# Optimization experiments

Measured on AMD Instinct MI355X. Metric: run time of the kernel, lower is better.

The kernel has to match this reference:

```python
import jax, jax.numpy as jnp
import numpy as np


def setup_inputs() -> dict:
    key = jax.random.key(0)
    k0, k1, k2, k3 = jax.random.split(key, 4)
    T, H, I, E, K = 2048, 2048, 1408, 8, 2  # tokens, hidden, intermediate, experts, top-k
    hidden_states = jax.random.normal(k0, (T, H), dtype=jnp.float32)
    router_weight = jax.random.normal(k1, (H, E), dtype=jnp.float32) * 0.02
    gate_up_weight = jax.random.normal(k2, (E, H, 2 * I), dtype=jnp.float32) * 0.02
    down_weight = jax.random.normal(k3, (E, I, H), dtype=jnp.float32) * 0.02
    return {
        "hidden_states": hidden_states,
        "router_weight": router_weight,
        "gate_up_weight": gate_up_weight,
        "down_weight": down_weight,
        "top_k": K,
    }


def reference(hidden_states, router_weight, gate_up_weight, down_weight, top_k):
    # Router: logits -> softmax -> top-k -> renormalize ('normalization' path)
    router_logits = hidden_states @ router_weight                  # [T, E]
    router_weights = jax.nn.softmax(router_logits, axis=-1)       # [T, E]
    topk_w, topk_idx = jax.lax.top_k(router_weights, top_k)       # [T, K]
    topk_w = topk_w / jnp.sum(topk_w, axis=-1, keepdims=True)     # router_weights_topk_reduced

    T, H = hidden_states.shape
    I = down_weight.shape[1]

    # Grouped gate_up GEMM (dense-per-expert reference for the grouped GMM)
    gate_up = jnp.einsum('th,ehf->etf', hidden_states, gate_up_weight)  # [E, T, 2I]
    gate, up = gate_up[..., :I], gate_up[..., I:]
    swish_out = jax.nn.silu(gate) * up                              # SWIGLU  [E, T, I]
    mlp_out = jnp.einsum('eti,eih->eth', swish_out, down_weight)    # [E, T, H]

    # Scatter-combine: gather each token's top-k expert outputs, weighted sum
    sel = mlp_out[topk_idx, jnp.arange(T)[:, None]]                 # [T, K, H]
    out = jnp.sum(sel * topk_w[..., None], axis=1)                  # [T, H]
    return out
```

## Files before the change

kernel.cpp:

```cpp
#include <hip/hip_runtime.h>
#include <hip/hip_bf16.h>
#include <math.h>

#define T_TOK 2048
#define HDIM  2048
#define IDIM  1408
#define NG    2816
#define NEXP  8
#define NPAIR (T_TOK*2)
#define RPAD  6144

typedef __attribute__((ext_vector_type(4))) float  f32x4;
typedef __attribute__((ext_vector_type(4))) short  s16x4;
typedef __attribute__((ext_vector_type(8))) short  s16x8;
typedef __attribute__((ext_vector_type(8))) __bf16 bf16x8;

__device__ __forceinline__ short f2bf(float f) {
  union { float f; unsigned u; } v; v.f = f;
  unsigned r = v.u + 0x7FFFu + ((v.u >> 16) & 1u);
  return (short)(r >> 16);
}

__device__ __forceinline__ float bf2f(short s) {
  union { unsigned u; float f; } v; v.u = ((unsigned)(unsigned short)s) << 16;
  return v.f;
}

__device__ __forceinline__ void gload_lds16(const void* g, void* l) {
  __builtin_amdgcn_global_load_lds((const __attribute__((address_space(1))) unsigned int*)g,
                                   (__attribute__((address_space(3))) unsigned int*)l,
                                   16, 0, 0);
}

__global__ void router_kernel(const float* __restrict__ hs, const float* __restrict__ rw,
                              int* __restrict__ pair_e, float* __restrict__ pair_w,
                              int* __restrict__ pair_pos, int* __restrict__ counts) {
  int wid = threadIdx.x >> 6, lane = threadIdx.x & 63;
  int t = blockIdx.x * 4 + wid;
  float acc[NEXP];
#pragma unroll
  for (int e = 0; e < NEXP; e++) acc[e] = 0.f;
  const float* h = hs + (size_t)t * HDIM;
  for (int k = lane; k < HDIM; k += 64) {
    float x = h[k];
    f32x4 w0 = *(const f32x4*)(rw + (size_t)k * NEXP);
    f32x4 w1 = *(const f32x4*)(rw + (size_t)k * NEXP + 4);
#pragma unroll
    for (int e = 0; e < 4; e++) { acc[e] += x * w0[e]; acc[e + 4] += x * w1[e]; }
  }
#pragma unroll
  for (int e = 0; e < NEXP; e++)
#pragma unroll
    for (int off = 32; off > 0; off >>= 1)
      acc[e] += __shfl_xor(acc[e], off, 64);
  if (lane == 0) {
    int i1 = 0; float v1 = acc[0];
#pragma unroll
    for (int e = 1; e < NEXP; e++) if (acc[e] > v1) { v1 = acc[e]; i1 = e; }
    int i2 = -1; float v2 = -3.4e38f;
#pragma unroll
    for (int e = 0; e < NEXP; e++) if (e != i1 && acc[e] > v2) { v2 = acc[e]; i2 = e; }
    float w2 = 1.f / (1.f + expf(v1 - v2));
    float w1 = 1.f - w2;
    int p1 = atomicAdd(&counts[i1], 1);
    int p2 = atomicAdd(&counts[i2], 1);
    pair_e[2*t]   = i1; pair_w[2*t]   = w1; pair_pos[2*t]   = p1;
    pair_e[2*t+1] = i2; pair_w[2*t+1] = w2; pair_pos[2*t+1] = p2;
  }
}

__global__ void prefix_kernel(const int* __restrict__ counts, int* __restrict__ offs) {
  if (threadIdx.x == 0) {
    int s = 0;
    for (int e = 0; e < NEXP; e++) { offs[e] = s; s += (counts[e] + 255) & ~255; }
    offs[NEXP] = s;
  }
}

__global__ void rowmap_kernel(const int* __restrict__ pair_e, const float* __restrict__ pair_w,
                              const int* __restrict__ pair_pos, const int* __restrict__ offs,
                              int* __restrict__ row_token, float* __restrict__ row_weight,
                              int* __restrict__ tok2row) {
  int p = blockIdx.x * 256 + threadIdx.x;
  if (p >= NPAIR) return;
  int e = pair_e[p];
  int row = offs[e] + pair_pos[p];
  row_token[row] = p >> 1;
  row_weight[row] = pair_w[p];
  tok2row[p] = row;
}

__global__ __launch_bounds__(256) void gather_kernel(const float* __restrict__ hs,
                                                     const int* __restrict__ row_token,
                                                     short* __restrict__ A_c) {
  int r = blockIdx.x;
  int tok = row_token[r];
  int t = threadIdx.x;
  if (tok < 0) {
    *(s16x8*)&A_c[(size_t)r * HDIM + t * 8] = (s16x8)0;
    return;
  }
  const float* src = hs + (size_t)tok * HDIM + t * 8;
  f32x4 v0 = *(const f32x4*)src;
  f32x4 v1 = *(const f32x4*)(src + 4);
  s16x8 o;
#pragma unroll
  for (int j = 0; j < 4; j++) { o[j] = f2bf(v0[j]); o[4 + j] = f2bf(v1[j]); }
  int dstg = (t & ~7) | ((t & 7) ^ (r & 7));
  *(s16x8*)&A_c[(size_t)r * HDIM + dstg * 8] = o;
}

__global__ __launch_bounds__(512, 2) void gateup_kernel(
    const short* __restrict__ A_c, const float* __restrict__ guw,
    const int* __restrict__ offs, short* __restrict__ S) {
  int nb = blockIdx.x;
  int rb = blockIdx.y * 256;
  if (rb >= offs[NEXP]) return;
  int e = 0;
#pragma unroll
  for (int i = 1; i < NEXP; i++) e += (rb >= offs[i]);
  const float* Wsrc = guw + (size_t)e * HDIM * NG;
  const short* Ar = A_c + (size_t)rb * HDIM;

  __shared__ short bufA[2][256 * 64];
  __shared__ short bufB[256 * 64];
  int tid = threadIdx.x, lane = tid & 63, wid = tid >> 6;
  int wm = wid >> 2, wn = wid & 3;
  int lm = lane & 15, lg = lane >> 4;

  int oct = tid >> 4, kq = tid & 15;
  int n0 = oct * 8;
  int col = (n0 < 128) ? (nb * 128 + n0) : (IDIM + nb * 128 + (n0 - 128));
  const float* Bp = Wsrc + col;

  f32x4 acc[8][4];
#pragma unroll
  for (int a = 0; a < 8; a++)
#pragma unroll
    for (int b = 0; b < 4; b++) acc[a][b] = (f32x4)0.f;

  f32x4 va[4], vb[4];

  auto STAGE_A = [&](int buf, int kt) {
    int k0 = kt * 64;
#pragma unroll
    for (int it = 0; it < 4; it++) {
      int idx = tid + it * 512;
      gload_lds16(Ar + (size_t)(idx >> 3) * HDIM + k0 + (idx & 7) * 8, &bufA[buf][idx * 8]);
    }
  };
  auto LOAD_B = [&](int kt) {
    const float* p = Bp + (size_t)(kt * 64 + kq * 4) * NG;
#pragma unroll
    for (int j = 0; j < 4; j++) {
      va[j] = *(const f32x4*)(p + (size_t)j * NG);
      vb[j] = *(const f32x4*)(p + (size_t)j * NG + 4);
    }
  };
  auto WRITE_B = [&]() {
    int gc = kq >> 1, half = kq & 1;
#pragma unroll
    for (int i = 0; i < 8; i++) {
      int n = n0 + i;
      s16x4 w;
#pragma unroll
      for (int j = 0; j < 4; j++) w[j] = f2bf(i < 4 ? va[j][i] : vb[j][i - 4]);
      *(s16x4*)&bufB[n * 64 + ((gc ^ (n & 7)) * 8) + half * 4] = w;
    }
  };

  STAGE_A(0, 0);
  LOAD_B(0);
  const int NT = HDIM / 64;
#pragma unroll 1
  for (int kt = 0; kt < NT; kt++) {
    int cur = kt & 1;
    if (kt + 1 < NT) {
      STAGE_A(cur ^ 1, kt + 1);
      asm volatile("s_waitcnt vmcnt(4)" ::: "memory");
    } else {
      asm volatile("s_waitcnt vmcnt(0)" ::: "memory");
    }
    WRITE_B();
    if (kt + 1 < NT) LOAD_B(kt + 1);
    asm volatile("s_waitcnt lgkmcnt(0)" ::: "memory");
    __builtin_amdgcn_s_barrier();
#pragma unroll
    for (int ks = 0; ks < 2; ks++) {
      bf16x8 a[8], b[4];
#pragma unroll
      for (int mi = 0; mi < 8; mi++) {
        int m = wm * 128 + mi * 16 + lm;
        a[mi] = *(const bf16x8*)&bufA[cur][m * 64 + (((ks * 4 + lg) ^ (m & 7)) * 8)];
      }
#pragma unroll
      for (int nf = 0; nf < 4; nf++) {
        int n = (nf >> 1) * 128 + wn * 32 + (nf & 1) * 16 + lm;
        b[nf] = *(const bf16x8*)&bufB[n * 64 + (((ks * 4 + lg) ^ (n & 7)) * 8)];
      }
      __builtin_amdgcn_s_setprio(1);
#pragma unroll
      for (int mi = 0; mi < 8; mi++)
#pragma unroll
        for (int nf = 0; nf < 4; nf++)
          acc[mi][nf] = __builtin_amdgcn_mfma_f32_16x16x32_bf16(a[mi], b[nf], acc[mi][nf], 0, 0, 0);
      __builtin_amdgcn_s_setprio(0);
    }
    asm volatile("s_waitcnt lgkmcnt(0)" ::: "memory");
    __builtin_amdgcn_s_barrier();
  }
#pragma unroll
  for (int mi = 0; mi < 8; mi++)
#pragma unroll
    for (int nfg = 0; nfg < 2; nfg++)
#pragma unroll
      for (int j = 0; j < 4; j++) {
        int row = wm * 128 + mi * 16 + lg * 4 + j;
        int rg = rb + row;
        int scol = nb * 128 + wn * 32 + nfg * 16 + lm;
        int base = scol & ~63, o = scol & 63;
        int dc = (((o >> 3) ^ (rg & 7)) << 3) | (o & 7);
        float g = acc[mi][nfg][j], u = acc[mi][nfg + 2][j];
        float sv = (g / (1.f + expf(-g))) * u;
        S[(size_t)rg * IDIM + base + dc] = f2bf(sv);
      }
}

__global__ __launch_bounds__(512, 2) void down_kernel(
    const short* __restrict__ S, const float* __restrict__ dw,
    const int* __restrict__ offs, short* __restrict__ Sout) {
  int nb = blockIdx.x;
  int rb = blockIdx.y * 256;
  if (rb >= offs[NEXP]) return;
  int e = 0;
#pragma unroll
  for (int i = 1; i < NEXP; i++) e += (rb >= offs[i]);
  const float* Wsrc = dw + (size_t)e * IDIM * HDIM;
  const short* Ar = S + (size_t)rb * IDIM;

  __shared__ short bufA[2][256 * 64];
  __shared__ short bufB[256 * 64];
  int tid = threadIdx.x, lane = tid & 63, wid = tid >> 6;
  int wm = wid >> 2, wn = wid & 3;
  int lm = lane & 15, lg = lane >> 4;

  int oct = tid >> 4, kq = tid & 15;
  int n0 = oct * 8;
  const float* Bp = Wsrc + nb * 256 + n0;

  f32x4 acc[8][4];
#pragma unroll
  for (int a = 0; a < 8; a++)
#pragma unroll
    for (int b = 0; b < 4; b++) acc[a][b] = (f32x4)0.f;

  f32x4 va[4], vb[4];

  auto STAGE_A = [&](int buf, int kt) {
    int k0 = kt * 64;
#pragma unroll
    for (int it = 0; it < 4; it++) {
      int idx = tid + it * 512;
      gload_lds16(Ar + (size_t)(idx >> 3) * IDIM + k0 + (idx & 7) * 8, &bufA[buf][idx * 8]);
    }
  };
  auto LOAD_B = [&](int kt) {
    const float* p = Bp + (size_t)(kt * 64 + kq * 4) * HDIM;
#pragma unroll
    for (int j = 0; j < 4; j++) {
      va[j] = *(const f32x4*)(p + (size_t)j * HDIM);
      vb[j] = *(const f32x4*)(p + (size_t)j * HDIM + 4);
    }
  };
  auto WRITE_B = [&]() {
    int gc = kq >> 1, half = kq & 1;
#pragma unroll
    for (int i = 0; i < 8; i++) {
      int n = n0 + i;
      s16x4 w;
#pragma unroll
      for (int j = 0; j < 4; j++) w[j] = f2bf(i < 4 ? va[j][i] : vb[j][i - 4]);
      *(s16x4*)&bufB[n * 64 + ((gc ^ (n & 7)) * 8) + half * 4] = w;
    }
  };

  STAGE_A(0, 0);
  LOAD_B(0);
  const int NT = IDIM / 64;
#pragma unroll 1
  for (int kt = 0; kt < NT; kt++) {
    int cur = kt & 1;
    if (kt + 1 < NT) {
      STAGE_A(cur ^ 1, kt + 1);
      asm volatile("s_waitcnt vmcnt(4)" ::: "memory");
    } else {
      asm volatile("s_waitcnt vmcnt(0)" ::: "memory");
    }
    WRITE_B();
    if (kt + 1 < NT) LOAD_B(kt + 1);
    asm volatile("s_waitcnt lgkmcnt(0)" ::: "memory");
    __builtin_amdgcn_s_barrier();
#pragma unroll
    for (int ks = 0; ks < 2; ks++) {
      bf16x8 a[8], b[4];
#pragma unroll
      for (int mi = 0; mi < 8; mi++) {
        int m = wm * 128 + mi * 16 + lm;
        a[mi] = *(const bf16x8*)&bufA[cur][m * 64 + (((ks * 4 + lg) ^ (m & 7)) * 8)];
      }
#pragma unroll
      for (int nf = 0; nf < 4; nf++) {
        int n = wn * 64 + nf * 16 + lm;
        b[nf] = *(const bf16x8*)&bufB[n * 64 + (((ks * 4 + lg) ^ (n & 7)) * 8)];
      }
      __builtin_amdgcn_s_setprio(1);
#pragma unroll
      for (int mi = 0; mi < 8; mi++)
#pragma unroll
        for (int nf = 0; nf < 4; nf++)
          acc[mi][nf] = __builtin_amdgcn_mfma_f32_16x16x32_bf16(a[mi], b[nf], acc[mi][nf], 0, 0, 0);
      __builtin_amdgcn_s_setprio(0);
    }
    asm volatile("s_waitcnt lgkmcnt(0)" ::: "memory");
    __builtin_amdgcn_s_barrier();
  }
#pragma unroll
  for (int mi = 0; mi < 8; mi++)
#pragma unroll
    for (int nf = 0; nf < 4; nf++)
#pragma unroll
      for (int j = 0; j < 4; j++) {
        int row = wm * 128 + mi * 16 + lg * 4 + j;
        int col = nb * 256 + wn * 64 + nf * 16 + lm;
        Sout[(size_t)(rb + row) * HDIM + col] = f2bf(acc[mi][nf][j]);
      }
}

__global__ __launch_bounds__(256) void combine_kernel(
    const short* __restrict__ Sout, const int* __restrict__ tok2row,
    const float* __restrict__ row_weight, float* __restrict__ out) {
  int t = blockIdx.x;
  int r1 = tok2row[2 * t], r2 = tok2row[2 * t + 1];
  float w1 = row_weight[r1], w2 = row_weight[r2];
  int c = threadIdx.x * 8;
  s16x8 a = *(const s16x8*)&Sout[(size_t)r1 * HDIM + c];
  s16x8 b = *(const s16x8*)&Sout[(size_t)r2 * HDIM + c];
  float* o = out + (size_t)t * HDIM + c;
#pragma unroll
  for (int j = 0; j < 8; j++) o[j] = w1 * bf2f(a[j]) + w2 * bf2f(b[j]);
}

extern "C" void kernel_launch(void* const* d_in, const int* in_sizes, int n_in,
                              void* d_out, int out_size, void* d_ws, size_t ws_size,
                              hipStream_t stream) {
  const float* hs  = (const float*)d_in[0];
  const float* rw  = (const float*)d_in[1];
  const float* guw = (const float*)d_in[2];
  const float* dw  = (const float*)d_in[3];
  float* out = (float*)d_out;

  char* ws = (char*)d_ws;
  size_t off = 0;
  auto take = [&](size_t b) { size_t p = off; off = (off + b + 255) & ~(size_t)255; return p; };
  size_t s_off      = take((size_t)RPAD * IDIM * 2);
  int*   counts     = (int*)(ws + take(32 * 4));
  int*   offs       = (int*)(ws + take(16 * 4));
  int*   pair_e     = (int*)(ws + take(NPAIR * 4));
  float* pair_w     = (float*)(ws + take(NPAIR * 4));
  int*   pair_pos   = (int*)(ws + take(NPAIR * 4));
  int*   row_token  = (int*)(ws + take(RPAD * 4));
  float* row_weight = (float*)(ws + take(RPAD * 4));
  int*   tok2row    = (int*)(ws + take(NPAIR * 4));
  size_t ac_off     = take((size_t)RPAD * HDIM * 2);
  size_t sout_off   = take((size_t)RPAD * HDIM * 2);

  short* S    = (short*)(ws + s_off);
  short* A_c  = (short*)(ws + ac_off);
  short* Sout = (short*)(ws + sout_off);

  hipMemsetAsync(counts, 0, 32 * 4, stream);
  hipMemsetAsync(row_token, 0xFF, RPAD * 4, stream);

  router_kernel<<<T_TOK / 4, 256, 0, stream>>>(hs, rw, pair_e, pair_w, pair_pos, counts);
  prefix_kernel<<<1, 64, 0, stream>>>(counts, offs);
  rowmap_kernel<<<NPAIR / 256, 256, 0, stream>>>(pair_e, pair_w, pair_pos, offs,
                                                 row_token, row_weight, tok2row);
  gather_kernel<<<RPAD, 256, 0, stream>>>(hs, row_token, A_c);

  gateup_kernel<<<dim3(11, RPAD / 256), 512, 0, stream>>>(A_c, guw, offs, S);
  down_kernel<<<dim3(8, RPAD / 256), 512, 0, stream>>>(S, dw, offs, Sout);
  combine_kernel<<<T_TOK, 256, 0, stream>>>(Sout, tok2row, row_weight, out);
}
```

Before: 288.9 us.

## Double-buffer B tiles in LDS and overlap conversion with MFMA

Both GEMM kernels now keep two LDS buffers for the bf16-converted weight tile. The fp32-to-bf16 conversion and LDS write of the next B tile move between the two MFMA k-substeps, and global B loads are issued two tiles ahead. This takes the B conversion and its barrier-protected LDS write off the critical path before each tile's MFMAs. In exchange, LDS per block grows from about 96KB to 128KB and the weight prefetch registers stay live longer.

```diff
diff --git a/kernel.cpp b/kernel.cpp
--- a/kernel.cpp
+++ b/kernel.cpp
@@ -123,7 +123,7 @@
   const short* Ar = A_c + (size_t)rb * HDIM;
 
   __shared__ short bufA[2][256 * 64];
-  __shared__ short bufB[256 * 64];
+  __shared__ short bufB[2][256 * 64];
   int tid = threadIdx.x, lane = tid & 63, wid = tid >> 6;
   int wm = wid >> 2, wn = wid & 3;
   int lm = lane & 15, lg = lane >> 4;
@@ -157,7 +157,7 @@
       vb[j] = *(const f32x4*)(p + (size_t)j * NG + 4);
     }
   };
-  auto WRITE_B = [&]() {
+  auto WRITE_B = [&](int buf) {
     int gc = kq >> 1, half = kq & 1;
 #pragma unroll
     for (int i = 0; i < 8; i++) {
@@ -165,47 +165,53 @@
       s16x4 w;
 #pragma unroll
       for (int j = 0; j < 4; j++) w[j] = f2bf(i < 4 ? va[j][i] : vb[j][i - 4]);
-      *(s16x4*)&bufB[n * 64 + ((gc ^ (n & 7)) * 8) + half * 4] = w;
-    }
+      *(s16x4*)&bufB[buf][n * 64 + ((gc ^ (n & 7)) * 8) + half * 4] = w;
+    }
+  };
+  auto MFMA_KS = [&](int cur, int ks) {
+    bf16x8 a[8], b[4];
+#pragma unroll
+    for (int mi = 0; mi < 8; mi++) {
+      int m = wm * 128 + mi * 16 + lm;
+      a[mi] = *(const bf16x8*)&bufA[cur][m * 64 + (((ks * 4 + lg) ^ (m & 7)) * 8)];
+    }
+#pragma unroll
+    for (int nf = 0; nf < 4; nf++) {
+      int n = (nf >> 1) * 128 + wn * 32 + (nf & 1) * 16 + lm;
+      b[nf] = *(const bf16x8*)&bufB[cur][n * 64 + (((ks * 4 + lg) ^ (n & 7)) * 8)];
+    }
+    __builtin_amdgcn_s_setprio(1);
+#pragma unroll
+    for (int mi = 0; mi < 8; mi++)
+#pragma unroll
+      for (int nf = 0; nf < 4; nf++)
+        acc[mi][nf] = __builtin_amdgcn_mfma_f32_16x16x32_bf16(a[mi], b[nf], acc[mi][nf], 0, 0, 0);
+    __builtin_amdgcn_s_setprio(0);
   };
 
   STAGE_A(0, 0);
   LOAD_B(0);
+  WRITE_B(0);
+  LOAD_B(1);
+  asm volatile("s_waitcnt lgkmcnt(0)" ::: "memory");
+
   const int NT = HDIM / 64;
 #pragma unroll 1
   for (int kt = 0; kt < NT; kt++) {
     int cur = kt & 1;
     if (kt + 1 < NT) {
       STAGE_A(cur ^ 1, kt + 1);
-      asm volatile("s_waitcnt vmcnt(4)" ::: "memory");
+      asm volatile("s_waitcnt vmcnt(12)" ::: "memory");
     } else {
       asm volatile("s_waitcnt vmcnt(0)" ::: "memory");
     }
-    WRITE_B();
-    if (kt + 1 < NT) LOAD_B(kt + 1);
-    asm volatile("s_waitcnt lgkmcnt(0)" ::: "memory");
     __builtin_amdgcn_s_barrier();
-#pragma unroll
-    for (int ks = 0; ks < 2; ks++) {
-      bf16x8 a[8], b[4];
-#pragma unroll
-      for (int mi = 0; mi < 8; mi++) {
-        int m = wm * 128 + mi * 16 + lm;
-        a[mi] = *(const bf16x8*)&bufA[cur][m * 64 + (((ks * 4 + lg) ^ (m & 7)) * 8)];
-      }
-#pragma unroll
-      for (int nf = 0; nf < 4; nf++) {
-        int n = (nf >> 1) * 128 + wn * 32 + (nf & 1) * 16 + lm;
-        b[nf] = *(const bf16x8*)&bufB[n * 64 + (((ks * 4 + lg) ^ (n & 7)) * 8)];
-      }
-      __builtin_amdgcn_s_setprio(1);
-#pragma unroll
-      for (int mi = 0; mi < 8; mi++)
-#pragma unroll
-        for (int nf = 0; nf < 4; nf++)
-          acc[mi][nf] = __builtin_amdgcn_mfma_f32_16x16x32_bf16(a[mi], b[nf], acc[mi][nf], 0, 0, 0);
-      __builtin_amdgcn_s_setprio(0);
-    }
+    MFMA_KS(cur, 0);
+    if (kt + 1 < NT) {
+      WRITE_B(cur ^ 1);
+      if (kt + 2 < NT) LOAD_B(kt + 2);
+    }
+    MFMA_KS(cur, 1);
     asm volatile("s_waitcnt lgkmcnt(0)" ::: "memory");
     __builtin_amdgcn_s_barrier();
   }
@@ -239,7 +245,7 @@
   const short* Ar = S + (size_t)rb * IDIM;
 
   __shared__ short bufA[2][256 * 64];
-  __shared__ short bufB[256 * 64];
+  __shared__ short bufB[2][256 * 64];
   int tid = threadIdx.x, lane = tid & 63, wid = tid >> 6;
   int wm = wid >> 2, wn = wid & 3;
   int lm = lane & 15, lg = lane >> 4;
@@ -272,7 +278,7 @@
       vb[j] = *(const f32x4*)(p + (size_t)j * HDIM + 4);
     }
   };
-  auto WRITE_B = [&]() {
+  auto WRITE_B = [&](int buf) {
     int gc = kq >> 1, half = kq & 1;
 #pragma unroll
     for (int i = 0; i < 8; i++) {
@@ -280,47 +286,53 @@
       s16x4 w;
 #pragma unroll
       for (int j = 0; j < 4; j++) w[j] = f2bf(i < 4 ? va[j][i] : vb[j][i - 4]);
-      *(s16x4*)&bufB[n * 64 + ((gc ^ (n & 7)) * 8) + half * 4] = w;
-    }
+      *(s16x4*)&bufB[buf][n * 64 + ((gc ^ (n & 7)) * 8) + half * 4] = w;
+    }
+  };
+  auto MFMA_KS = [&](int cur, int ks) {
+    bf16x8 a[8], b[4];
+#pragma unroll
+    for (int mi = 0; mi < 8; mi++) {
+      int m = wm * 128 + mi * 16 + lm;
+      a[mi] = *(const bf16x8*)&bufA[cur][m * 64 + (((ks * 4 + lg) ^ (m & 7)) * 8)];
+    }
+#pragma unroll
+    for (int nf = 0; nf < 4; nf++) {
+      int n = wn * 64 + nf * 16 + lm;
+      b[nf] = *(const bf16x8*)&bufB[cur][n * 64 + (((ks * 4 + lg) ^ (n & 7)) * 8)];
+    }
+    __builtin_amdgcn_s_setprio(1);
+#pragma unroll
+    for (int mi = 0; mi < 8; mi++)
+#pragma unroll
+      for (int nf = 0; nf < 4; nf++)
+        acc[mi][nf] = __builtin_amdgcn_mfma_f32_16x16x32_bf16(a[mi], b[nf], acc[mi][nf], 0, 0, 0);
+    __builtin_amdgcn_s_setprio(0);
   };
 
   STAGE_A(0, 0);
   LOAD_B(0);
+  WRITE_B(0);
+  LOAD_B(1);
+  asm volatile("s_waitcnt lgkmcnt(0)" ::: "memory");
+
   const int NT = IDIM / 64;
 #pragma unroll 1
   for (int kt = 0; kt < NT; kt++) {
     int cur = kt & 1;
     if (kt + 1 < NT) {
       STAGE_A(cur ^ 1, kt + 1);
-      asm volatile("s_waitcnt vmcnt(4)" ::: "memory");
+      asm volatile("s_waitcnt vmcnt(12)" ::: "memory");
     } else {
       asm volatile("s_waitcnt vmcnt(0)" ::: "memory");
     }
-    WRITE_B();
-    if (kt + 1 < NT) LOAD_B(kt + 1);
-    asm volatile("s_waitcnt lgkmcnt(0)" ::: "memory");
     __builtin_amdgcn_s_barrier();
-#pragma unroll
-    for (int ks = 0; ks < 2; ks++) {
-      bf16x8 a[8], b[4];
-#pragma unroll
-      for (int mi = 0; mi < 8; mi++) {
-        int m = wm * 128 + mi * 16 + lm;
-        a[mi] = *(const bf16x8*)&bufA[cur][m * 64 + (((ks * 4 + lg) ^ (m & 7)) * 8)];
-      }
-#pragma unroll
-      for (int nf = 0; nf < 4; nf++) {
-        int n = wn * 64 + nf * 16 + lm;
-        b[nf] = *(const bf16x8*)&bufB[n * 64 + (((ks * 4 + lg) ^ (n & 7)) * 8)];
-      }
-      __builtin_amdgcn_s_setprio(1);
-#pragma unroll
-      for (int mi = 0; mi < 8; mi++)
-#pragma unroll
-        for (int nf = 0; nf < 4; nf++)
-          acc[mi][nf] = __builtin_amdgcn_mfma_f32_16x16x32_bf16(a[mi], b[nf], acc[mi][nf], 0, 0, 0);
-      __builtin_amdgcn_s_setprio(0);
-    }
+    MFMA_KS(cur, 0);
+    if (kt + 1 < NT) {
+      WRITE_B(cur ^ 1);
+      if (kt + 2 < NT) LOAD_B(kt + 2);
+    }
+    MFMA_KS(cur, 1);
     asm volatile("s_waitcnt lgkmcnt(0)" ::: "memory");
     __builtin_amdgcn_s_barrier();
   }
```

Result: no change. 285.8 us (-1.0%).

## Shrink grouped GEMM tiles to 128x128, cut expert padding, remap blocks per XCD

Applied to the files above, without the earlier changes.

Switches both grouped GEMMs from 256x256 tiles with 512 threads to 128x128 tiles with 256 threads and three blocks per CU. Expert padding drops from 256 to 128 rows, and RPAD shrinks with it, so less padded work is computed. Blocks are launched on a 1D grid whose index is remapped so neighbouring work items land on the same XCD. The finely tuned vmcnt-overlapped pipeline is replaced by plain __syncthreads around WRITE_B, and smaller tiles give less data reuse per load, so there is a risk of extra global traffic and exposed latency.

```diff
diff --git a/kernel.cpp b/kernel.cpp
--- a/kernel.cpp
+++ b/kernel.cpp
@@ -8,7 +8,7 @@
 #define NG    2816
 #define NEXP  8
 #define NPAIR (T_TOK*2)
-#define RPAD  6144
+#define RPAD  5120
 
 typedef __attribute__((ext_vector_type(4))) float  f32x4;
 typedef __attribute__((ext_vector_type(4))) short  s16x4;
@@ -72,7 +72,7 @@
 __global__ void prefix_kernel(const int* __restrict__ counts, int* __restrict__ offs) {
   if (threadIdx.x == 0) {
     int s = 0;
-    for (int e = 0; e < NEXP; e++) { offs[e] = s; s += (counts[e] + 255) & ~255; }
+    for (int e = 0; e < NEXP; e++) { offs[e] = s; s += (counts[e] + 127) & ~127; }
     offs[NEXP] = s;
   }
 }
@@ -110,11 +110,13 @@
   *(s16x8*)&A_c[(size_t)r * HDIM + dstg * 8] = o;
 }
 
-__global__ __launch_bounds__(512, 2) void gateup_kernel(
+__global__ __launch_bounds__(256, 3) void gateup_kernel(
     const short* __restrict__ A_c, const float* __restrict__ guw,
     const int* __restrict__ offs, short* __restrict__ S) {
-  int nb = blockIdx.x;
-  int rb = blockIdx.y * 256;
+  int bid = blockIdx.x;
+  int work = (bid & 7) * 110 + (bid >> 3);
+  int rblk = work / 22, nb = work % 22;
+  int rb = rblk * 128;
   if (rb >= offs[NEXP]) return;
   int e = 0;
 #pragma unroll
@@ -122,20 +124,20 @@
   const float* Wsrc = guw + (size_t)e * HDIM * NG;
   const short* Ar = A_c + (size_t)rb * HDIM;
 
-  __shared__ short bufA[2][256 * 64];
-  __shared__ short bufB[256 * 64];
+  __shared__ short As[2][128 * 64];
+  __shared__ short Bs[128 * 64];
   int tid = threadIdx.x, lane = tid & 63, wid = tid >> 6;
-  int wm = wid >> 2, wn = wid & 3;
+  int wm = wid >> 1, wn = wid & 1;
   int lm = lane & 15, lg = lane >> 4;
 
   int oct = tid >> 4, kq = tid & 15;
   int n0 = oct * 8;
-  int col = (n0 < 128) ? (nb * 128 + n0) : (IDIM + nb * 128 + (n0 - 128));
-  const float* Bp = Wsrc + col;
-
-  f32x4 acc[8][4];
-#pragma unroll
-  for (int a = 0; a < 8; a++)
+  int gcol = (oct < 8) ? (nb * 64 + n0) : (IDIM + nb * 64 + (n0 - 64));
+  const float* Bp = Wsrc + gcol;
+
+  f32x4 acc[4][4];
+#pragma unroll
+  for (int a = 0; a < 4; a++)
 #pragma unroll
     for (int b = 0; b < 4; b++) acc[a][b] = (f32x4)0.f;
 
@@ -145,8 +147,8 @@
     int k0 = kt * 64;
 #pragma unroll
     for (int it = 0; it < 4; it++) {
-      int idx = tid + it * 512;
-      gload_lds16(Ar + (size_t)(idx >> 3) * HDIM + k0 + (idx & 7) * 8, &bufA[buf][idx * 8]);
+      int idx = tid + it * 256;
+      gload_lds16(Ar + (size_t)(idx >> 3) * HDIM + k0 + (idx & 7) * 8, &As[buf][idx * 8]);
     }
   };
   auto LOAD_B = [&](int kt) {
@@ -165,7 +167,7 @@
       s16x4 w;
 #pragma unroll
       for (int j = 0; j < 4; j++) w[j] = f2bf(i < 4 ? va[j][i] : vb[j][i - 4]);
-      *(s16x4*)&bufB[n * 64 + ((gc ^ (n & 7)) * 8) + half * 4] = w;
+      *(s16x4*)&Bs[n * 64 + ((gc ^ (n & 7)) * 8) + half * 4] = w;
     }
   };
 
@@ -175,62 +177,58 @@
 #pragma unroll 1
   for (int kt = 0; kt < NT; kt++) {
     int cur = kt & 1;
+    __syncthreads();
+    WRITE_B();
+    __syncthreads();
     if (kt + 1 < NT) {
       STAGE_A(cur ^ 1, kt + 1);
-      asm volatile("s_waitcnt vmcnt(4)" ::: "memory");
-    } else {
-      asm volatile("s_waitcnt vmcnt(0)" ::: "memory");
-    }
-    WRITE_B();
-    if (kt + 1 < NT) LOAD_B(kt + 1);
-    asm volatile("s_waitcnt lgkmcnt(0)" ::: "memory");
-    __builtin_amdgcn_s_barrier();
+      LOAD_B(kt + 1);
+    }
 #pragma unroll
     for (int ks = 0; ks < 2; ks++) {
-      bf16x8 a[8], b[4];
-#pragma unroll
-      for (int mi = 0; mi < 8; mi++) {
-        int m = wm * 128 + mi * 16 + lm;
-        a[mi] = *(const bf16x8*)&bufA[cur][m * 64 + (((ks * 4 + lg) ^ (m & 7)) * 8)];
+      bf16x8 a[4], b[4];
+#pragma unroll
+      for (int mi = 0; mi < 4; mi++) {
+        int m = wm * 64 + mi * 16 + lm;
+        a[mi] = *(const bf16x8*)&As[cur][m * 64 + (((ks * 4 + lg) ^ (m & 7)) * 8)];
       }
 #pragma unroll
       for (int nf = 0; nf < 4; nf++) {
-        int n = (nf >> 1) * 128 + wn * 32 + (nf & 1) * 16 + lm;
-        b[nf] = *(const bf16x8*)&bufB[n * 64 + (((ks * 4 + lg) ^ (n & 7)) * 8)];
+        int n = (nf >> 1) * 64 + wn * 32 + (nf & 1) * 16 + lm;
+        b[nf] = *(const bf16x8*)&Bs[n * 64 + (((ks * 4 + lg) ^ (n & 7)) * 8)];
       }
       __builtin_amdgcn_s_setprio(1);
 #pragma unroll
-      for (int mi = 0; mi < 8; mi++)
+      for (int mi = 0; mi < 4; mi++)
 #pragma unroll
         for (int nf = 0; nf < 4; nf++)
           acc[mi][nf] = __builtin_amdgcn_mfma_f32_16x16x32_bf16(a[mi], b[nf], acc[mi][nf], 0, 0, 0);
       __builtin_amdgcn_s_setprio(0);
     }
-    asm volatile("s_waitcnt lgkmcnt(0)" ::: "memory");
-    __builtin_amdgcn_s_barrier();
-  }
-#pragma unroll
-  for (int mi = 0; mi < 8; mi++)
-#pragma unroll
-    for (int nfg = 0; nfg < 2; nfg++)
-#pragma unroll
-      for (int j = 0; j < 4; j++) {
-        int row = wm * 128 + mi * 16 + lg * 4 + j;
+  }
+#pragma unroll
+  for (int mi = 0; mi < 4; mi++)
+#pragma unroll
+    for (int j = 0; j < 2; j++)
+#pragma unroll
+      for (int jj = 0; jj < 4; jj++) {
+        int row = wm * 64 + mi * 16 + lg * 4 + jj;
         int rg = rb + row;
-        int scol = nb * 128 + wn * 32 + nfg * 16 + lm;
-        int base = scol & ~63, o = scol & 63;
+        int o = wn * 32 + j * 16 + lm;
         int dc = (((o >> 3) ^ (rg & 7)) << 3) | (o & 7);
-        float g = acc[mi][nfg][j], u = acc[mi][nfg + 2][j];
+        float g = acc[mi][j][jj], u = acc[mi][2 + j][jj];
         float sv = (g / (1.f + expf(-g))) * u;
-        S[(size_t)rg * IDIM + base + dc] = f2bf(sv);
-      }
-}
-
-__global__ __launch_bounds__(512, 2) void down_kernel(
+        S[(size_t)rg * IDIM + nb * 64 + dc] = f2bf(sv);
+      }
+}
+
+__global__ __launch_bounds__(256, 3) void down_kernel(
     const short* __restrict__ S, const float* __restrict__ dw,
     const int* __restrict__ offs, short* __restrict__ Sout) {
-  int nb = blockIdx.x;
-  int rb = blockIdx.y * 256;
+  int bid = blockIdx.x;
+  int work = (bid & 7) * 80 + (bid >> 3);
+  int rblk = work / 16, nb = work % 16;
+  int rb = rblk * 128;
   if (rb >= offs[NEXP]) return;
   int e = 0;
 #pragma unroll
@@ -238,19 +236,19 @@
   const float* Wsrc = dw + (size_t)e * IDIM * HDIM;
   const short* Ar = S + (size_t)rb * IDIM;
 
-  __shared__ short bufA[2][256 * 64];
-  __shared__ short bufB[256 * 64];
+  __shared__ short As[2][128 * 64];
+  __shared__ short Bs[128 * 64];
   int tid = threadIdx.x, lane = tid & 63, wid = tid >> 6;
-  int wm = wid >> 2, wn = wid & 3;
+  int wm = wid >> 1, wn = wid & 1;
   int lm = lane & 15, lg = lane >> 4;
 
   int oct = tid >> 4, kq = tid & 15;
   int n0 = oct * 8;
-  const float* Bp = Wsrc + nb * 256 + n0;
-
-  f32x4 acc[8][4];
-#pragma unroll
-  for (int a = 0; a < 8; a++)
+  const float* Bp = Wsrc + nb * 128 + n0;
+
+  f32x4 acc[4][4];
+#pragma unroll
+  for (int a = 0; a < 4; a++)
 #pragma unroll
     for (int b = 0; b < 4; b++) acc[a][b] = (f32x4)0.f;
 
@@ -260,8 +258,8 @@
     int k0 = kt * 64;
 #pragma unroll
     for (int it = 0; it < 4; it++) {
-      int idx = tid + it * 512;
-      gload_lds16(Ar + (size_t)(idx >> 3) * IDIM + k0 + (idx & 7) * 8, &bufA[buf][idx * 8]);
+      int idx = tid + it * 256;
+      gload_lds16(Ar + (size_t)(idx >> 3) * IDIM + k0 + (idx & 7) * 8, &As[buf][idx * 8]);
     }
   };
   auto LOAD_B = [&](int kt) {
@@ -280,7 +278,7 @@
       s16x4 w;
 #pragma unroll
       for (int j = 0; j < 4; j++) w[j] = f2bf(i < 4 ? va[j][i] : vb[j][i - 4]);
-      *(s16x4*)&bufB[n * 64 + ((gc ^ (n & 7)) * 8) + half * 4] = w;
+      *(s16x4*)&Bs[n * 64 + ((gc ^ (n & 7)) * 8) + half * 4] = w;
     }
   };
 
@@ -290,49 +288,44 @@
 #pragma unroll 1
   for (int kt = 0; kt < NT; kt++) {
     int cur = kt & 1;
+    __syncthreads();
+    WRITE_B();
+    __syncthreads();
     if (kt + 1 < NT) {
       STAGE_A(cur ^ 1, kt + 1);
-      asm volatile("s_waitcnt vmcnt(4)" ::: "memory");
-    } else {
-      asm volatile("s_waitcnt vmcnt(0)" ::: "memory");
-    }
-    WRITE_B();
-    if (kt + 1 < NT) LOAD_B(kt + 1);
-    asm volatile("s_waitcnt lgkmcnt(0)" ::: "memory");
-    __builtin_amdgcn_s_barrier();
+      LOAD_B(kt + 1);
+    }
 #pragma unroll
     for (int ks = 0; ks < 2; ks++) {
-      bf16x8 a[8], b[4];
-#pragma unroll
-      for (int mi = 0; mi < 8; mi++) {
-        int m = wm * 128 + mi * 16 + lm;
-        a[mi] = *(const bf16x8*)&bufA[cur][m * 64 + (((ks * 4 + lg) ^ (m & 7)) * 8)];
+      bf16x8 a[4], b[4];
+#pragma unroll
+      for (int mi = 0; mi < 4; mi++) {
+        int m = wm * 64 + mi * 16 + lm;
+        a[mi] = *(const bf16x8*)&As[cur][m * 64 + (((ks * 4 + lg) ^ (m & 7)) * 8)];
       }
 #pragma unroll
       for (int nf = 0; nf < 4; nf++) {
         int n = wn * 64 + nf * 16 + lm;
-        b[nf] = *(const bf16x8*)&bufB[n * 64 + (((ks * 4 + lg) ^ (n & 7)) * 8)];
+        b[nf] = *(const bf16x8*)&Bs[n * 64 + (((ks * 4 + lg) ^ (n & 7)) * 8)];
       }
       __builtin_amdgcn_s_setprio(1);
 #pragma unroll
-      for (int mi = 0; mi < 8; mi++)
+      for (int mi = 0; mi < 4; mi++)
 #pragma unroll
         for (int nf = 0; nf < 4; nf++)
           acc[mi][nf] = __builtin_amdgcn_mfma_f32_16x16x32_bf16(a[mi], b[nf], acc[mi][nf], 0, 0, 0);
       __builtin_amdgcn_s_setprio(0);
     }
-    asm volatile("s_waitcnt lgkmcnt(0)" ::: "memory");
-    __builtin_amdgcn_s_barrier();
-  }
-#pragma unroll
-  for (int mi = 0; mi < 8; mi++)
+  }
+#pragma unroll
+  for (int mi = 0; mi < 4; mi++)
 #pragma unroll
     for (int nf = 0; nf < 4; nf++)
 #pragma unroll
-      for (int j = 0; j < 4; j++) {
-        int row = wm * 128 + mi * 16 + lg * 4 + j;
-        int col = nb * 256 + wn * 64 + nf * 16 + lm;
-        Sout[(size_t)(rb + row) * HDIM + col] = f2bf(acc[mi][nf][j]);
+      for (int jj = 0; jj < 4; jj++) {
+        int row = wm * 64 + mi * 16 + lg * 4 + jj;
+        int col = nb * 128 + wn * 64 + nf * 16 + lm;
+        Sout[(size_t)(rb + row) * HDIM + col] = f2bf(acc[mi][nf][jj]);
       }
 }
 
@@ -387,7 +380,7 @@
                                                  row_token, row_weight, tok2row);
   gather_kernel<<<RPAD, 256, 0, stream>>>(hs, row_token, A_c);
 
-  gateup_kernel<<<dim3(11, RPAD / 256), 512, 0, stream>>>(A_c, guw, offs, S);
-  down_kernel<<<dim3(8, RPAD / 256), 512, 0, stream>>>(S, dw, offs, Sout);
+  gateup_kernel<<<880, 256, 0, stream>>>(A_c, guw, offs, S);
+  down_kernel<<<640, 256, 0, stream>>>(S, dw, offs, Sout);
   combine_kernel<<<T_TOK, 256, 0, stream>>>(Sout, tok2row, row_weight, out);
 }
```

Result: slower. 342.5 us (+18.6%).

## Convert down weights to bf16 inside gateup kernel and simplify down GEMM

Applied to the files above, without the earlier changes.

The gateup kernel now also converts the fp32 down-projection weights into a transposed, swizzled bf16 buffer. Active blocks interleave this conversion with their MFMA loop, and inactive blocks spend their slot doing only conversion. The down kernel is rewritten to use 128x128 tiles with 256 threads, loads both operands directly to LDS as bf16, and remaps block ids across experts. This removes the per-tile fp32-to-bf16 conversion of the down weights and halves their read traffic in that kernel. In exchange it adds register pressure and extra memory traffic to gateup, and the new down kernel has a single-buffered loop with full syncthreads barriers.

```diff
diff --git a/kernel.cpp b/kernel.cpp
--- a/kernel.cpp
+++ b/kernel.cpp
@@ -9,6 +9,8 @@
 #define NEXP  8
 #define NPAIR (T_TOK*2)
 #define RPAD  6144
+#define DW_GRANULES (NEXP*HDIM*(IDIM/8))
+#define CVT_Q 11264
 
 typedef __attribute__((ext_vector_type(4))) float  f32x4;
 typedef __attribute__((ext_vector_type(4))) short  s16x4;
@@ -112,10 +114,46 @@
 
 __global__ __launch_bounds__(512, 2) void gateup_kernel(
     const short* __restrict__ A_c, const float* __restrict__ guw,
-    const int* __restrict__ offs, short* __restrict__ S) {
+    const float* __restrict__ dwsrc, const int* __restrict__ offs,
+    short* __restrict__ S, short* __restrict__ Wd) {
   int nb = blockIdx.x;
   int rb = blockIdx.y * 256;
-  if (rb >= offs[NEXP]) return;
+  int bid = blockIdx.y * 11 + nb;
+  int tid = threadIdx.x;
+
+  float cf[8];
+  int cvt_h = 0, cvt_gk = 0, cvt_e = 0, cvt_ok = 0;
+  auto CVT_LOAD = [&](int kt) {
+    cvt_ok = 0;
+    if (tid < 352) {
+      int gid = bid * CVT_Q + kt * 352 + tid;
+      if (gid < DW_GRANULES) {
+        cvt_ok = 1;
+        cvt_h = gid & (HDIM - 1);
+        int rest = gid >> 11;
+        cvt_gk = rest % (IDIM / 8);
+        cvt_e = rest / (IDIM / 8);
+        const float* sp = dwsrc + ((size_t)cvt_e * IDIM + cvt_gk * 8) * HDIM + cvt_h;
+#pragma unroll
+        for (int j = 0; j < 8; j++) cf[j] = sp[(size_t)j * HDIM];
+      }
+    }
+  };
+  auto CVT_STORE = [&]() {
+    if (cvt_ok) {
+      int slot = (cvt_gk & ~7) | ((cvt_gk ^ cvt_h) & 7);
+      s16x8 o;
+#pragma unroll
+      for (int j = 0; j < 8; j++) o[j] = f2bf(cf[j]);
+      *(s16x8*)&Wd[((size_t)cvt_e * HDIM + cvt_h) * IDIM + slot * 8] = o;
+    }
+  };
+
+  bool active = (rb < offs[NEXP]);
+  if (!active) {
+    for (int kt = 0; kt < 32; kt++) { CVT_LOAD(kt); CVT_STORE(); }
+    return;
+  }
   int e = 0;
 #pragma unroll
   for (int i = 1; i < NEXP; i++) e += (rb >= offs[i]);
@@ -124,7 +162,7 @@
 
   __shared__ short bufA[2][256 * 64];
   __shared__ short bufB[256 * 64];
-  int tid = threadIdx.x, lane = tid & 63, wid = tid >> 6;
+  int lane = tid & 63, wid = tid >> 6;
   int wm = wid >> 2, wn = wid & 3;
   int lm = lane & 15, lg = lane >> 4;
 
@@ -167,6 +205,26 @@
       for (int j = 0; j < 4; j++) w[j] = f2bf(i < 4 ? va[j][i] : vb[j][i - 4]);
       *(s16x4*)&bufB[n * 64 + ((gc ^ (n & 7)) * 8) + half * 4] = w;
     }
+  };
+  auto MFMA_KS = [&](int cur, int ks) {
+    bf16x8 a[8], b[4];
+#pragma unroll
+    for (int mi = 0; mi < 8; mi++) {
+      int m = wm * 128 + mi * 16 + lm;
+      a[mi] = *(const bf16x8*)&bufA[cur][m * 64 + (((ks * 4 + lg) ^ (m & 7)) * 8)];
+    }
+#pragma unroll
+    for (int nf = 0; nf < 4; nf++) {
+      int n = (nf >> 1) * 128 + wn * 32 + (nf & 1) * 16 + lm;
+      b[nf] = *(const bf16x8*)&bufB[n * 64 + (((ks * 4 + lg) ^ (n & 7)) * 8)];
+    }
+    __builtin_amdgcn_s_setprio(1);
+#pragma unroll
+    for (int mi = 0; mi < 8; mi++)
+#pragma unroll
+      for (int nf = 0; nf < 4; nf++)
+        acc[mi][nf] = __builtin_amdgcn_mfma_f32_16x16x32_bf16(a[mi], b[nf], acc[mi][nf], 0, 0, 0);
+    __builtin_amdgcn_s_setprio(0);
   };
 
   STAGE_A(0, 0);
@@ -175,9 +233,10 @@
 #pragma unroll 1
   for (int kt = 0; kt < NT; kt++) {
     int cur = kt & 1;
+    CVT_LOAD(kt);
     if (kt + 1 < NT) {
       STAGE_A(cur ^ 1, kt + 1);
-      asm volatile("s_waitcnt vmcnt(4)" ::: "memory");
+      asm volatile("s_waitcnt vmcnt(12)" ::: "memory");
     } else {
       asm volatile("s_waitcnt vmcnt(0)" ::: "memory");
     }
@@ -185,27 +244,9 @@
     if (kt + 1 < NT) LOAD_B(kt + 1);
     asm volatile("s_waitcnt lgkmcnt(0)" ::: "memory");
     __builtin_amdgcn_s_barrier();
-#pragma unroll
-    for (int ks = 0; ks < 2; ks++) {
-      bf16x8 a[8], b[4];
-#pragma unroll
-      for (int mi = 0; mi < 8; mi++) {
-        int m = wm * 128 + mi * 16 + lm;
-        a[mi] = *(const bf16x8*)&bufA[cur][m * 64 + (((ks * 4 + lg) ^ (m & 7)) * 8)];
-      }
-#pragma unroll
-      for (int nf = 0; nf < 4; nf++) {
-        int n = (nf >> 1) * 128 + wn * 32 + (nf & 1) * 16 + lm;
-        b[nf] = *(const bf16x8*)&bufB[n * 64 + (((ks * 4 + lg) ^ (n & 7)) * 8)];
-      }
-      __builtin_amdgcn_s_setprio(1);
-#pragma unroll
-      for (int mi = 0; mi < 8; mi++)
-#pragma unroll
-        for (int nf = 0; nf < 4; nf++)
-          acc[mi][nf] = __builtin_amdgcn_mfma_f32_16x16x32_bf16(a[mi], b[nf], acc[mi][nf], 0, 0, 0);
-      __builtin_amdgcn_s_setprio(0);
-    }
+    MFMA_KS(cur, 0);
+    MFMA_KS(cur, 1);
+    CVT_STORE();
     asm volatile("s_waitcnt lgkmcnt(0)" ::: "memory");
     __builtin_amdgcn_s_barrier();
   }
@@ -226,113 +267,71 @@
       }
 }
 
-__global__ __launch_bounds__(512, 2) void down_kernel(
-    const short* __restrict__ S, const float* __restrict__ dw,
+__global__ __launch_bounds__(256) void down_kernel(
+    const short* __restrict__ S, const short* __restrict__ Wd,
     const int* __restrict__ offs, short* __restrict__ Sout) {
-  int nb = blockIdx.x;
-  int rb = blockIdx.y * 256;
+  int bid = blockIdx.x;
+  int work = (bid & 7) * 96 + (bid >> 3);
+  int rblk = work / 16, nb = work % 16;
+  int rb = rblk * 128;
   if (rb >= offs[NEXP]) return;
   int e = 0;
 #pragma unroll
   for (int i = 1; i < NEXP; i++) e += (rb >= offs[i]);
-  const float* Wsrc = dw + (size_t)e * IDIM * HDIM;
   const short* Ar = S + (size_t)rb * IDIM;
-
-  __shared__ short bufA[2][256 * 64];
-  __shared__ short bufB[256 * 64];
+  const short* Bw = Wd + ((size_t)e * HDIM + nb * 128) * IDIM;
+
+  __shared__ short As[128 * 64];
+  __shared__ short Bs[128 * 64];
   int tid = threadIdx.x, lane = tid & 63, wid = tid >> 6;
-  int wm = wid >> 2, wn = wid & 3;
+  int wm = wid >> 1, wn = wid & 1;
   int lm = lane & 15, lg = lane >> 4;
 
-  int oct = tid >> 4, kq = tid & 15;
-  int n0 = oct * 8;
-  const float* Bp = Wsrc + nb * 256 + n0;
-
-  f32x4 acc[8][4];
-#pragma unroll
-  for (int a = 0; a < 8; a++)
+  f32x4 acc[4][4];
+#pragma unroll
+  for (int a = 0; a < 4; a++)
 #pragma unroll
     for (int b = 0; b < 4; b++) acc[a][b] = (f32x4)0.f;
 
-  f32x4 va[4], vb[4];
-
-  auto STAGE_A = [&](int buf, int kt) {
+  for (int kt = 0; kt < IDIM / 64; kt++) {
     int k0 = kt * 64;
+    __syncthreads();
 #pragma unroll
     for (int it = 0; it < 4; it++) {
-      int idx = tid + it * 512;
-      gload_lds16(Ar + (size_t)(idx >> 3) * IDIM + k0 + (idx & 7) * 8, &bufA[buf][idx * 8]);
-    }
-  };
-  auto LOAD_B = [&](int kt) {
-    const float* p = Bp + (size_t)(kt * 64 + kq * 4) * HDIM;
-#pragma unroll
-    for (int j = 0; j < 4; j++) {
-      va[j] = *(const f32x4*)(p + (size_t)j * HDIM);
-      vb[j] = *(const f32x4*)(p + (size_t)j * HDIM + 4);
-    }
-  };
-  auto WRITE_B = [&]() {
-    int gc = kq >> 1, half = kq & 1;
-#pragma unroll
-    for (int i = 0; i < 8; i++) {
-      int n = n0 + i;
-      s16x4 w;
-#pragma unroll
-      for (int j = 0; j < 4; j++) w[j] = f2bf(i < 4 ? va[j][i] : vb[j][i - 4]);
-      *(s16x4*)&bufB[n * 64 + ((gc ^ (n & 7)) * 8) + half * 4] = w;
-    }
-  };
-
-  STAGE_A(0, 0);
-  LOAD_B(0);
-  const int NT = IDIM / 64;
-#pragma unroll 1
-  for (int kt = 0; kt < NT; kt++) {
-    int cur = kt & 1;
-    if (kt + 1 < NT) {
-      STAGE_A(cur ^ 1, kt + 1);
-      asm volatile("s_waitcnt vmcnt(4)" ::: "memory");
-    } else {
-      asm volatile("s_waitcnt vmcnt(0)" ::: "memory");
-    }
-    WRITE_B();
-    if (kt + 1 < NT) LOAD_B(kt + 1);
-    asm volatile("s_waitcnt lgkmcnt(0)" ::: "memory");
-    __builtin_amdgcn_s_barrier();
+      int idx = tid + it * 256;
+      gload_lds16(Ar + (size_t)(idx >> 3) * IDIM + k0 + (idx & 7) * 8, &As[idx * 8]);
+      gload_lds16(Bw + (size_t)(idx >> 3) * IDIM + k0 + (idx & 7) * 8, &Bs[idx * 8]);
+    }
+    __syncthreads();
 #pragma unroll
     for (int ks = 0; ks < 2; ks++) {
-      bf16x8 a[8], b[4];
-#pragma unroll
-      for (int mi = 0; mi < 8; mi++) {
-        int m = wm * 128 + mi * 16 + lm;
-        a[mi] = *(const bf16x8*)&bufA[cur][m * 64 + (((ks * 4 + lg) ^ (m & 7)) * 8)];
+      bf16x8 a[4], b[4];
+#pragma unroll
+      for (int mi = 0; mi < 4; mi++) {
+        int m = wm * 64 + mi * 16 + lm;
+        a[mi] = *(const bf16x8*)&As[m * 64 + (((ks * 4 + lg) ^ (m & 7)) * 8)];
       }
 #pragma unroll
       for (int nf = 0; nf < 4; nf++) {
         int n = wn * 64 + nf * 16 + lm;
-        b[nf] = *(const bf16x8*)&bufB[n * 64 + (((ks * 4 + lg) ^ (n & 7)) * 8)];
-      }
-      __builtin_amdgcn_s_setprio(1);
-#pragma unroll
-      for (int mi = 0; mi < 8; mi++)
+        b[nf] = *(const bf16x8*)&Bs[n * 64 + (((ks * 4 + lg) ^ (n & 7)) * 8)];
+      }
+#pragma unroll
+      for (int mi = 0; mi < 4; mi++)
 #pragma unroll
         for (int nf = 0; nf < 4; nf++)
           acc[mi][nf] = __builtin_amdgcn_mfma_f32_16x16x32_bf16(a[mi], b[nf], acc[mi][nf], 0, 0, 0);
-      __builtin_amdgcn_s_setprio(0);
-    }
-    asm volatile("s_waitcnt lgkmcnt(0)" ::: "memory");
-    __builtin_amdgcn_s_barrier();
-  }
-#pragma unroll
-  for (int mi = 0; mi < 8; mi++)
+    }
+  }
+#pragma unroll
+  for (int mi = 0; mi < 4; mi++)
 #pragma unroll
     for (int nf = 0; nf < 4; nf++)
 #pragma unroll
-      for (int j = 0; j < 4; j++) {
-        int row = wm * 128 + mi * 16 + lg * 4 + j;
-        int col = nb * 256 + wn * 64 + nf * 16 + lm;
-        Sout[(size_t)(rb + row) * HDIM + col] = f2bf(acc[mi][nf][j]);
+      for (int jj = 0; jj < 4; jj++) {
+        int row = wm * 64 + mi * 16 + lg * 4 + jj;
+        int col = nb * 128 + wn * 64 + nf * 16 + lm;
+        Sout[(size_t)(rb + row) * HDIM + col] = f2bf(acc[mi][nf][jj]);
       }
 }
 
@@ -373,10 +372,12 @@
   int*   tok2row    = (int*)(ws + take(NPAIR * 4));
   size_t ac_off     = take((size_t)RPAD * HDIM * 2);
   size_t sout_off   = take((size_t)RPAD * HDIM * 2);
+  size_t wd_off     = take((size_t)NEXP * HDIM * IDIM * 2);
 
   short* S    = (short*)(ws + s_off);
   short* A_c  = (short*)(ws + ac_off);
   short* Sout = (short*)(ws + sout_off);
+  short* Wd   = (short*)(ws + wd_off);
 
   hipMemsetAsync(counts, 0, 32 * 4, stream);
   hipMemsetAsync(row_token, 0xFF, RPAD * 4, stream);
@@ -387,7 +388,7 @@
                                                  row_token, row_weight, tok2row);
   gather_kernel<<<RPAD, 256, 0, stream>>>(hs, row_token, A_c);
 
-  gateup_kernel<<<dim3(11, RPAD / 256), 512, 0, stream>>>(A_c, guw, offs, S);
-  down_kernel<<<dim3(8, RPAD / 256), 512, 0, stream>>>(S, dw, offs, Sout);
+  gateup_kernel<<<dim3(11, RPAD / 256), 512, 0, stream>>>(A_c, guw, dw, offs, S, Wd);
+  down_kernel<<<768, 256, 0, stream>>>(S, Wd, offs, Sout);
   combine_kernel<<<T_TOK, 256, 0, stream>>>(Sout, tok2row, row_weight, out);
 }
```

Result: no change. 284.9 us (-1.4%).
